# Performance work log

Hardware: AMD Instinct MI355X
Metric: run time of the kernel (lower is better)

Reference implementation:

```python
import jax, jax.numpy as jnp
import numpy as np

N, E, H, HEADS = 50000, 800000, 64, 4
EPS = 1e-5
NEG_SLOPE = 0.2


def _ln(x, g, b):
    mu = x.mean(-1, keepdims=True)
    var = x.var(-1, keepdims=True)
    return (x - mu) / jnp.sqrt(var + EPS) * g + b


def _gat(x, row, col, W, a_src, a_dst, bias, heads, out_dim, concat):
    # PyG GATConv: add self-loops, linear, per-edge attention, segment softmax, scatter-agg
    n = x.shape[0]
    loop = jnp.arange(n, dtype=row.dtype)
    r = jnp.concatenate([row, loop])  # message sources
    c = jnp.concatenate([col, loop])  # message targets (aggregation index)
    h = (x @ W).reshape(n, heads, out_dim)              # [N, heads, out]
    a_s = jnp.sum(h * a_src, axis=-1)                   # [N, heads]
    a_d = jnp.sum(h * a_dst, axis=-1)                   # [N, heads]
    e = jax.nn.leaky_relu(a_s[r] + a_d[c], NEG_SLOPE)   # [E', heads]
    m = jax.ops.segment_max(e, c, num_segments=n)       # stable softmax per target node
    p = jnp.exp(e - m[c])
    alpha = p / jax.ops.segment_sum(p, c, num_segments=n)[c]
    out = jax.ops.segment_sum(h[r] * alpha[..., None], c, num_segments=n)  # [N, heads, out]
    out = out.reshape(n, heads * out_dim) if concat else out.mean(axis=1)
    return out + bias


def setup_inputs() -> dict:
    key = jax.random.key(0)
    ks = jax.random.split(key, 16)
    d = {}
    d["node_embeds"] = jax.random.normal(ks[0], (N, H), jnp.float32)
    d["edge_index"] = jax.random.randint(ks[1], (2, E), 0, N, jnp.int32)
    d["edge_embeds"] = jax.random.normal(ks[2], (E, H), jnp.float32)
    layer_cfg = [(H, HEADS, H, True), (H * HEADS, HEADS, H, True), (H * HEADS, 1, H, False)]
    i = 3
    for li, (din, heads, dout, concat) in enumerate(layer_cfg):
        d[f"W{li}"] = jax.random.normal(ks[i], (din, heads * dout), jnp.float32) * 0.05; i += 1
        d[f"asrc{li}"] = jax.random.normal(ks[i], (heads, dout), jnp.float32) * 0.05; i += 1
        d[f"adst{li}"] = jax.random.normal(ks[i], (heads, dout), jnp.float32) * 0.05; i += 1
        odim = heads * dout if concat else dout
        d[f"b{li}"] = jnp.zeros((odim,), jnp.float32)
        d[f"g{li}"] = jnp.ones((odim,), jnp.float32)
        d[f"be{li}"] = jnp.zeros((odim,), jnp.float32)
    return d


def reference(node_embeds, edge_index, edge_embeds,
              W0, asrc0, adst0, b0, g0, be0,
              W1, asrc1, adst1, b1, g1, be1,
              W2, asrc2, adst2, b2, g2, be2):
    row, col = edge_index[0], edge_index[1]
    # scatter-mean edge embeddings onto target nodes (reduce='mean', clamp count>=1)
    cnt = jnp.maximum(jax.ops.segment_sum(jnp.ones((E,), jnp.float32), col, num_segments=N), 1.0)
    x = node_embeds + jax.ops.segment_sum(edge_embeds, col, num_segments=N) / cnt[:, None]
    layers = [
        (W0, asrc0, adst0, b0, g0, be0, HEADS, True),
        (W1, asrc1, adst1, b1, g1, be1, HEADS, True),
        (W2, asrc2, adst2, b2, g2, be2, 1, False),
    ]
    for (W, a_s, a_d, b, g, be, heads, concat) in layers:
        x = _gat(x, row, col, W, a_s, a_d, b, heads, H, concat)
        x = jax.nn.elu(_ln(x, g, be))
        # dropout: identity in eval mode
    return x
```

## Files before the change

kernel.cpp:

```cpp
#include <hip/hip_runtime.h>
#include <math.h>

#define NN 50000
#define NE 800000
#define MPAD 50048
#define NB 196

typedef __attribute__((ext_vector_type(8))) short bf16x8;
typedef __attribute__((ext_vector_type(8))) unsigned short u16x8;
typedef __attribute__((ext_vector_type(4))) float f32x4;

__device__ __forceinline__ float leaky(float x){ return x > 0.f ? x : 0.2f*x; }

__device__ __forceinline__ unsigned short f2bf(float f){
  unsigned int u = __float_as_uint(f);
  unsigned int r = (u + 0x7fffu + ((u >> 16) & 1u)) >> 16;
  return (unsigned short)r;
}
__device__ __forceinline__ float bf2f(unsigned short u){
  return __uint_as_float(((unsigned int)u) << 16);
}

__global__ void k_zero(int* __restrict__ deg,
                       float* __restrict__ AS0, float* __restrict__ AD0,
                       float* __restrict__ AS1, float* __restrict__ AD1,
                       float* __restrict__ AS2, float* __restrict__ AD2){
  int i = blockIdx.x*blockDim.x + threadIdx.x;
  if (i < NN) deg[i] = 0;
  if (i < NN*4){
    AS0[i]=0.f; AD0[i]=0.f;
    AS1[i]=0.f; AD1[i]=0.f;
    AS2[i]=0.f; AD2[i]=0.f;
  }
}

__global__ void k_hist(const int* __restrict__ col, int* __restrict__ deg){
  int e = blockIdx.x*blockDim.x + threadIdx.x;
  if (e < NE) atomicAdd(&deg[col[e]], 1);
}

__global__ void k_scan1(const int* __restrict__ deg, int* __restrict__ off,
                        int* __restrict__ bsum){
  __shared__ int ws[4];
  int t = threadIdx.x;
  int i = blockIdx.x*256 + t;
  int v = (i<NN)? deg[i] : 0;
  int lane = t & 63, w = t >> 6;
  int x = v;
  #pragma unroll
  for (int d=1; d<64; d<<=1){
    int y = __shfl_up(x, d, 64);
    if (lane >= d) x += y;
  }
  if (lane==63) ws[w] = x;
  __syncthreads();
  int woff = 0;
  #pragma unroll
  for (int k=0;k<3;++k) if (k < w) woff += ws[k];
  int incl = x + woff;
  if (i<NN) off[i] = incl - v;
  if (t==255) bsum[blockIdx.x] = incl;
}

__global__ void k_scan2(int* __restrict__ bsum, int* __restrict__ off){
  __shared__ int ws[4];
  int t = threadIdx.x;
  int v = (t<NB)? bsum[t] : 0;
  int lane = t & 63, w = t >> 6;
  int x = v;
  #pragma unroll
  for (int d=1; d<64; d<<=1){
    int y = __shfl_up(x, d, 64);
    if (lane >= d) x += y;
  }
  if (lane==63) ws[w] = x;
  __syncthreads();
  int woff = 0;
  #pragma unroll
  for (int k=0;k<3;++k) if (k < w) woff += ws[k];
  int incl = x + woff;
  if (t<NB) bsum[t] = incl - v;
  if (t==NB-1) off[NN] = incl;
}

__global__ void k_scan3(const int* __restrict__ bsum, int* __restrict__ off,
                        int* __restrict__ cursor){
  int i = blockIdx.x*256 + threadIdx.x;
  if (i<NN){
    int v = off[i] + bsum[blockIdx.x];
    off[i] = v;
    cursor[i] = v;
  }
}

__global__ void k_scatter(const int* __restrict__ row, const int* __restrict__ col,
                          int* __restrict__ cursor, int* __restrict__ esrc, int* __restrict__ eid){
  int e = blockIdx.x*blockDim.x + threadIdx.x;
  if (e < NE){
    int c = col[e];
    int pos = atomicAdd(&cursor[c], 1);
    esrc[pos] = row[e];
    eid[pos]  = e;
  }
}

__global__ void k_premix(const float* __restrict__ node, const float* __restrict__ ee,
                         const int* __restrict__ off, const int* __restrict__ eid,
                         unsigned short* __restrict__ Xb){
  int wid  = (int)((blockIdx.x*blockDim.x + threadIdx.x) >> 6);
  int lane = threadIdx.x & 63;
  if (wid >= NN) return;
  int g  = lane >> 3;
  int l8 = lane & 7;
  int s0 = off[wid], s1 = off[wid+1];

  float a[8];
  #pragma unroll
  for (int v=0;v<8;++v) a[v]=0.f;
  for (int p = s0 + g; p < s1; p += 8){
    int ed = eid[p];
    const float4* rp = reinterpret_cast<const float4*>(ee + (size_t)ed*64 + l8*8);
    float4 h0 = rp[0], h1 = rp[1];
    a[0]+=h0.x; a[1]+=h0.y; a[2]+=h0.z; a[3]+=h0.w;
    a[4]+=h1.x; a[5]+=h1.y; a[6]+=h1.z; a[7]+=h1.w;
  }
  #pragma unroll
  for (int mk=8; mk<64; mk<<=1){
    #pragma unroll
    for (int v=0;v<8;++v) a[v] += __shfl_xor(a[v], mk, 64);
  }
  if (lane < 8){
    int dcnt = s1 - s0;
    float c = 1.f/(float)(dcnt > 1 ? dcnt : 1);
    const float4* np = reinterpret_cast<const float4*>(node + (size_t)wid*64 + l8*8);
    float4 n0 = np[0], n1 = np[1];
    float nv[8] = {n0.x,n0.y,n0.z,n0.w,n1.x,n1.y,n1.z,n1.w};
    u16x8 o;
    #pragma unroll
    for (int v=0;v<8;++v) o[v] = f2bf(nv[v] + a[v]*c);
    *reinterpret_cast<u16x8*>(Xb + (size_t)wid*64 + l8*8) = o;
  }
}

__global__ void k_wconv(const float* __restrict__ W, unsigned short* __restrict__ Wt,
                        int K, int Ncols){
  int idx = blockIdx.x*blockDim.x + threadIdx.x;
  if (idx < K*Ncols){
    int n = idx / K, k = idx - n*K;
    Wt[idx] = f2bf(W[(size_t)k*Ncols + n]);
  }
}

template<int BN, int K, int HEADS>
__global__ __launch_bounds__(256)
void k_gemm_mfma(const unsigned short* __restrict__ A,
                 const unsigned short* __restrict__ Bt,
                 unsigned short* __restrict__ C,
                 const float* __restrict__ asrc, const float* __restrict__ adst,
                 float* __restrict__ AS, float* __restrict__ AD, int Nc){
  constexpr int BM = 128, BK = 32;
  constexpr int WNT = BN/32;
  __shared__ __align__(16) unsigned short As[BM*BK];
  __shared__ __align__(16) unsigned short Bs[BN*BK];
  const int tid  = threadIdx.x;
  const int lane = tid & 63;
  const int wid  = tid >> 6;
  const int wr   = wid >> 1, wc = wid & 1;
  const int bm   = blockIdx.y * BM, bn = blockIdx.x * BN;
  const int r    = lane >> 2, kq = lane & 3;

  f32x4 acc[4][WNT];
  #pragma unroll
  for (int i=0;i<4;++i)
    #pragma unroll
    for (int j=0;j<WNT;++j) acc[i][j] = (f32x4){0.f,0.f,0.f,0.f};

  for (int k0=0; k0<K; k0+=BK){
    #pragma unroll
    for (int i=0;i<2;++i){
      int arow = wid*32 + i*16 + r;
      __builtin_amdgcn_global_load_lds(
        (const __attribute__((address_space(1))) void*)(A + (size_t)(bm+arow)*K + k0 + kq*8),
        (__attribute__((address_space(3))) void*)&As[(wid*32 + i*16)*BK],
        16, 0, 0);
    }
    #pragma unroll
    for (int i=0;i<BN/64;++i){
      int brow = wid*(BN/4) + i*16 + r;
      __builtin_amdgcn_global_load_lds(
        (const __attribute__((address_space(1))) void*)(Bt + (size_t)(bn+brow)*K + k0 + kq*8),
        (__attribute__((address_space(3))) void*)&Bs[(wid*(BN/4) + i*16)*BK],
        16, 0, 0);
    }
    __syncthreads();

    bf16x8 af[4], bfr[WNT];
    #pragma unroll
    for (int mi=0; mi<4; ++mi)
      af[mi] = *reinterpret_cast<const bf16x8*>(&As[(wr*64 + mi*16 + (lane&15))*BK + (lane>>4)*8]);
    #pragma unroll
    for (int ni=0; ni<WNT; ++ni)
      bfr[ni] = *reinterpret_cast<const bf16x8*>(&Bs[(wc*(BN/2) + ni*16 + (lane&15))*BK + (lane>>4)*8]);
    #pragma unroll
    for (int mi=0; mi<4; ++mi)
      #pragma unroll
      for (int ni=0; ni<WNT; ++ni)
        acc[mi][ni] = __builtin_amdgcn_mfma_f32_16x16x32_bf16(af[mi], bfr[ni], acc[mi][ni], 0, 0, 0);
    __syncthreads();
  }

  const int head = (bn + wc*(BN/2)) >> 6;
  float av[WNT], dv[WNT];
  #pragma unroll
  for (int ni=0; ni<WNT; ++ni){
    int ccol = bn + wc*(BN/2) + ni*16 + (lane&15);
    av[ni] = asrc[ccol];
    dv[ni] = adst[ccol];
  }

  #pragma unroll
  for (int mi=0; mi<4; ++mi){
    #pragma unroll
    for (int ni=0; ni<WNT; ++ni){
      int ccol = bn + wc*(BN/2) + ni*16 + (lane&15);
      int rbase = bm + wr*64 + mi*16 + (lane>>4)*4;
      #pragma unroll
      for (int reg=0; reg<4; ++reg)
        C[(size_t)(rbase+reg)*Nc + ccol] = f2bf(acc[mi][ni][reg]);
    }
    float sp[4] = {0.f,0.f,0.f,0.f}, dp[4] = {0.f,0.f,0.f,0.f};
    #pragma unroll
    for (int ni=0; ni<WNT; ++ni)
      #pragma unroll
      for (int reg=0; reg<4; ++reg){
        sp[reg] += acc[mi][ni][reg]*av[ni];
        dp[reg] += acc[mi][ni][reg]*dv[ni];
      }
    #pragma unroll
    for (int reg=0; reg<4; ++reg)
      #pragma unroll
      for (int mk=1; mk<16; mk<<=1){
        sp[reg] += __shfl_xor(sp[reg], mk, 64);
        dp[reg] += __shfl_xor(dp[reg], mk, 64);
      }
    if ((lane & 15) == 0){
      int rr = bm + wr*64 + mi*16 + (lane>>4)*4;
      #pragma unroll
      for (int reg=0; reg<4; ++reg){
        atomicAdd(&AS[(size_t)(rr+reg)*HEADS + head], sp[reg]);
        atomicAdd(&AD[(size_t)(rr+reg)*HEADS + head], dp[reg]);
      }
    }
  }
}

template<int HEADS, bool OUT_BF16>
__global__ void k_agg(const unsigned short* __restrict__ Hb, const float* __restrict__ AS,
                      const float* __restrict__ AD, const int* __restrict__ off,
                      const int* __restrict__ esrc,
                      const float* __restrict__ bias, const float* __restrict__ gamma,
                      const float* __restrict__ beta, void* __restrict__ OutP){
  constexpr int D  = HEADS*64;
  constexpr int L  = (HEADS==4) ? 16 : 8;
  constexpr int C  = D / L;
  constexpr int NG = 64 / L;
  constexpr int NV = C / 8;
  int wid  = (int)((blockIdx.x*blockDim.x + threadIdx.x) >> 6);
  int lane = threadIdx.x & 63;
  if (wid >= NN) return;
  const int g    = lane / L;
  const int lrow = lane & (L-1);
  const int col0 = lrow * C;
  const int head = col0 >> 6;

  float ad    = AD[(size_t)wid*HEADS + head];
  float wself = leaky(AS[(size_t)wid*HEADS + head] + ad);
  int s0 = off[wid], s1 = off[wid+1];

  float m, psum;
  float acc[C];
  if (g == 0){
    m = wself; psum = 1.f;
    const u16x8* hp = reinterpret_cast<const u16x8*>(Hb + (size_t)wid*D + col0);
    u16x8 hv[NV];
    #pragma unroll
    for (int q=0;q<NV;++q) hv[q] = hp[q];
    #pragma unroll
    for (int v=0;v<C;++v) acc[v] = bf2f((unsigned short)hv[v>>3][v&7]);
  } else {
    m = -1e30f; psum = 0.f;
    #pragma unroll
    for (int v=0;v<C;++v) acc[v]=0.f;
  }

  for (int p = s0 + g; p < s1; p += NG){
    int src = esrc[p];
    float w = leaky(AS[(size_t)src*HEADS + head] + ad);
    float mn = fmaxf(m, w);
    float scale = __expf(m - mn);
    float pw    = __expf(w - mn);
    m = mn;
    psum = psum*scale + pw;
    const u16x8* hp = reinterpret_cast<const u16x8*>(Hb + (size_t)src*D + col0);
    u16x8 hv[NV];
    #pragma unroll
    for (int q=0;q<NV;++q) hv[q] = hp[q];
    #pragma unroll
    for (int v=0;v<C;++v) acc[v] = acc[v]*scale + pw*bf2f((unsigned short)hv[v>>3][v&7]);
  }

  #pragma unroll
  for (int mk=L; mk<64; mk<<=1){
    float m_o    = __shfl_xor(m, mk, 64);
    float psum_o = __shfl_xor(psum, mk, 64);
    float mn = fmaxf(m, m_o);
    float sA = __expf(m - mn);
    float sB = __expf(m_o - mn);
    psum = psum*sA + psum_o*sB;
    #pragma unroll
    for (int v=0;v<C;++v){
      float a_o = __shfl_xor(acc[v], mk, 64);
      acc[v] = acc[v]*sA + a_o*sB;
    }
    m = mn;
  }

  float inv = 1.f/psum;
  float val[C];
  float s=0.f, s2=0.f;
  #pragma unroll
  for (int v=0;v<C;++v){
    val[v] = acc[v]*inv + bias[col0+v];
    s  += val[v];
    s2 += val[v]*val[v];
  }
  #pragma unroll
  for (int mk=1; mk<64; mk<<=1){
    s  += __shfl_xor(s,  mk, 64);
    s2 += __shfl_xor(s2, mk, 64);
  }
  float mean = s/(float)(64*C);
  float var  = s2/(float)(64*C) - mean*mean;
  float rstd = rsqrtf(var + 1e-5f);
  if (g == 0){
    if constexpr (OUT_BF16){
      u16x8 o[NV];
      #pragma unroll
      for (int v=0;v<C;++v){
        float y = (val[v]-mean)*rstd*gamma[col0+v] + beta[col0+v];
        y = (y > 0.f) ? y : expm1f(y);
        o[v>>3][v&7] = f2bf(y);
      }
      u16x8* op = reinterpret_cast<u16x8*>((unsigned short*)OutP + (size_t)wid*D + col0);
      #pragma unroll
      for (int q=0;q<NV;++q) op[q] = o[q];
    } else {
      float o[C];
      #pragma unroll
      for (int v=0;v<C;++v){
        float y = (val[v]-mean)*rstd*gamma[col0+v] + beta[col0+v];
        o[v] = (y > 0.f) ? y : expm1f(y);
      }
      float4* op = reinterpret_cast<float4*>((float*)OutP + (size_t)wid*D + col0);
      #pragma unroll
      for (int q=0;q<C/4;++q){
        float4 o4 = {o[q*4+0],o[q*4+1],o[q*4+2],o[q*4+3]};
        op[q] = o4;
      }
    }
  }
}

extern "C" void kernel_launch(void* const* d_in, const int* in_sizes, int n_in,
                              void* d_out, int out_size, void* d_ws, size_t ws_size,
                              hipStream_t stream) {
  const float* node  = (const float*)d_in[0];
  const int*   eidx  = (const int*)d_in[1];
  const float* ee    = (const float*)d_in[2];
  const float* W0    = (const float*)d_in[3];
  const float* asrc0 = (const float*)d_in[4];
  const float* adst0 = (const float*)d_in[5];
  const float* b0    = (const float*)d_in[6];
  const float* g0    = (const float*)d_in[7];
  const float* be0   = (const float*)d_in[8];
  const float* W1    = (const float*)d_in[9];
  const float* asrc1 = (const float*)d_in[10];
  const float* adst1 = (const float*)d_in[11];
  const float* b1    = (const float*)d_in[12];
  const float* g1    = (const float*)d_in[13];
  const float* be1   = (const float*)d_in[14];
  const float* W2    = (const float*)d_in[15];
  const float* asrc2 = (const float*)d_in[16];
  const float* adst2 = (const float*)d_in[17];
  const float* b2    = (const float*)d_in[18];
  const float* g2    = (const float*)d_in[19];
  const float* be2   = (const float*)d_in[20];

  const int* row = eidx;
  const int* col = eidx + NE;

  unsigned short* Hb  = (unsigned short*)d_ws;
  unsigned short* Xb0 = Hb  + (size_t)MPAD*256;
  unsigned short* Xb  = Xb0 + (size_t)MPAD*64;
  unsigned short* Wt0 = Xb  + (size_t)MPAD*256;
  unsigned short* Wt1 = Wt0 + 256*64;
  unsigned short* Wt2 = Wt1 + 256*256;
  float* AS0 = (float*)(Wt2 + 64*256);
  float* AD0 = AS0 + (size_t)MPAD*4;
  float* AS1 = AD0 + (size_t)MPAD*4;
  float* AD1 = AS1 + (size_t)MPAD*4;
  float* AS2 = AD1 + (size_t)MPAD*4;
  float* AD2 = AS2 + (size_t)MPAD*4;
  int* deg   = (int*)(AD2 + (size_t)MPAD*4);
  int* off   = deg + NN;
  int* cursor= off + NN + 1;
  int* esrc  = cursor + NN;
  int* eid   = esrc + NE;
  int* bsum  = eid + NE;

  float* out = (float*)d_out;

  k_zero<<<(NN*4+255)/256, 256, 0, stream>>>(deg, AS0, AD0, AS1, AD1, AS2, AD2);
  k_hist<<<(NE+255)/256, 256, 0, stream>>>(col, deg);
  k_scan1<<<NB, 256, 0, stream>>>(deg, off, bsum);
  k_scan2<<<1, 256, 0, stream>>>(bsum, off);
  k_scan3<<<NB, 256, 0, stream>>>(bsum, off, cursor);
  k_scatter<<<(NE+255)/256, 256, 0, stream>>>(row, col, cursor, esrc, eid);

  k_wconv<<<(256*64 +255)/256, 256, 0, stream>>>(W0, Wt0, 64, 256);
  k_wconv<<<(256*256+255)/256, 256, 0, stream>>>(W1, Wt1, 256, 256);
  k_wconv<<<(64*256 +255)/256, 256, 0, stream>>>(W2, Wt2, 256, 64);

  int nwaveblk = (NN*64 + 255)/256;
  k_premix<<<nwaveblk, 256, 0, stream>>>(node, ee, off, eid, Xb0);

  {
    dim3 g(256/128, MPAD/128);
    k_gemm_mfma<128,64,4><<<g, 256, 0, stream>>>(Xb0, Wt0, Hb, asrc0, adst0, AS0, AD0, 256);
    k_agg<4,true><<<nwaveblk, 256, 0, stream>>>(Hb, AS0, AD0, off, esrc, b0, g0, be0, Xb);
  }
  {
    dim3 g(256/128, MPAD/128);
    k_gemm_mfma<128,256,4><<<g, 256, 0, stream>>>(Xb, Wt1, Hb, asrc1, adst1, AS1, AD1, 256);
    k_agg<4,true><<<nwaveblk, 256, 0, stream>>>(Hb, AS1, AD1, off, esrc, b1, g1, be1, Xb);
  }
  {
    dim3 g(64/64, MPAD/128);
    k_gemm_mfma<64,256,1><<<g, 256, 0, stream>>>(Xb, Wt2, Hb, asrc2, adst2, AS2, AD2, 64);
    k_agg<1,false><<<nwaveblk, 256, 0, stream>>>(Hb, AS2, AD2, off, esrc, b2, g2, be2, out);
  }
}
```

Before: 497.3 us.

## Precompute per-node softmax max in a pre-pass; drop online rescaling in aggregation

Adds a first pass in which the whole wave reads neighbor attention scores and reduces the per-head max. The main loop then accumulates exp(w-m) directly, with no running rescale, and the cross-group merge becomes a plain shuffle-add. It also halves lanes per row (L 16->8 and 8->4), so each lane holds more columns and more edge groups run in parallel. This costs an extra read of esrc and AS per node, and the wider per-lane accumulators raise register pressure.

```diff
diff --git a/kernel.cpp b/kernel.cpp
--- a/kernel.cpp
+++ b/kernel.cpp
@@ -261,7 +261,7 @@
                       const float* __restrict__ bias, const float* __restrict__ gamma,
                       const float* __restrict__ beta, void* __restrict__ OutP){
   constexpr int D  = HEADS*64;
-  constexpr int L  = (HEADS==4) ? 16 : 8;
+  constexpr int L  = (HEADS==4) ? 8 : 4;
   constexpr int C  = D / L;
   constexpr int NG = 64 / L;
   constexpr int NV = C / 8;
@@ -273,56 +273,82 @@
   const int col0 = lrow * C;
   const int head = col0 >> 6;
 
+  int s0 = off[wid], s1 = off[wid+1];
+
+  float m;
+  if constexpr (HEADS==4){
+    float4 ad4 = *reinterpret_cast<const float4*>(AD + (size_t)wid*4);
+    float4 as4 = *reinterpret_cast<const float4*>(AS + (size_t)wid*4);
+    float mx0 = leaky(as4.x+ad4.x), mx1 = leaky(as4.y+ad4.y);
+    float mx2 = leaky(as4.z+ad4.z), mx3 = leaky(as4.w+ad4.w);
+    for (int p = s0 + lane; p < s1; p += 64){
+      int src = esrc[p];
+      float4 a4 = *reinterpret_cast<const float4*>(AS + (size_t)src*4);
+      mx0 = fmaxf(mx0, leaky(a4.x+ad4.x));
+      mx1 = fmaxf(mx1, leaky(a4.y+ad4.y));
+      mx2 = fmaxf(mx2, leaky(a4.z+ad4.z));
+      mx3 = fmaxf(mx3, leaky(a4.w+ad4.w));
+    }
+    #pragma unroll
+    for (int mk=1; mk<64; mk<<=1){
+      mx0 = fmaxf(mx0, __shfl_xor(mx0, mk, 64));
+      mx1 = fmaxf(mx1, __shfl_xor(mx1, mk, 64));
+      mx2 = fmaxf(mx2, __shfl_xor(mx2, mk, 64));
+      mx3 = fmaxf(mx3, __shfl_xor(mx3, mk, 64));
+    }
+    float m01 = (head & 1) ? mx1 : mx0;
+    float m23 = (head & 1) ? mx3 : mx2;
+    m = (head & 2) ? m23 : m01;
+  } else {
+    float ad0 = AD[wid];
+    float mx0 = leaky(AS[wid]+ad0);
+    for (int p = s0 + lane; p < s1; p += 64){
+      int src = esrc[p];
+      mx0 = fmaxf(mx0, leaky(AS[src]+ad0));
+    }
+    #pragma unroll
+    for (int mk=1; mk<64; mk<<=1)
+      mx0 = fmaxf(mx0, __shfl_xor(mx0, mk, 64));
+    m = mx0;
+  }
+
   float ad    = AD[(size_t)wid*HEADS + head];
   float wself = leaky(AS[(size_t)wid*HEADS + head] + ad);
-  int s0 = off[wid], s1 = off[wid+1];
-
-  float m, psum;
+
+  float psum = 0.f;
   float acc[C];
+  #pragma unroll
+  for (int v=0;v<C;++v) acc[v]=0.f;
+
   if (g == 0){
-    m = wself; psum = 1.f;
+    float pw = __expf(wself - m);
+    psum = pw;
     const u16x8* hp = reinterpret_cast<const u16x8*>(Hb + (size_t)wid*D + col0);
     u16x8 hv[NV];
     #pragma unroll
     for (int q=0;q<NV;++q) hv[q] = hp[q];
     #pragma unroll
-    for (int v=0;v<C;++v) acc[v] = bf2f((unsigned short)hv[v>>3][v&7]);
-  } else {
-    m = -1e30f; psum = 0.f;
-    #pragma unroll
-    for (int v=0;v<C;++v) acc[v]=0.f;
+    for (int v=0;v<C;++v) acc[v] = pw*bf2f((unsigned short)hv[v>>3][v&7]);
   }
 
   for (int p = s0 + g; p < s1; p += NG){
     int src = esrc[p];
-    float w = leaky(AS[(size_t)src*HEADS + head] + ad);
-    float mn = fmaxf(m, w);
-    float scale = __expf(m - mn);
-    float pw    = __expf(w - mn);
-    m = mn;
-    psum = psum*scale + pw;
+    float w  = leaky(AS[(size_t)src*HEADS + head] + ad);
+    float pw = __expf(w - m);
+    psum += pw;
     const u16x8* hp = reinterpret_cast<const u16x8*>(Hb + (size_t)src*D + col0);
     u16x8 hv[NV];
     #pragma unroll
     for (int q=0;q<NV;++q) hv[q] = hp[q];
     #pragma unroll
-    for (int v=0;v<C;++v) acc[v] = acc[v]*scale + pw*bf2f((unsigned short)hv[v>>3][v&7]);
+    for (int v=0;v<C;++v) acc[v] += pw*bf2f((unsigned short)hv[v>>3][v&7]);
   }
 
   #pragma unroll
   for (int mk=L; mk<64; mk<<=1){
-    float m_o    = __shfl_xor(m, mk, 64);
-    float psum_o = __shfl_xor(psum, mk, 64);
-    float mn = fmaxf(m, m_o);
-    float sA = __expf(m - mn);
-    float sB = __expf(m_o - mn);
-    psum = psum*sA + psum_o*sB;
-    #pragma unroll
-    for (int v=0;v<C;++v){
-      float a_o = __shfl_xor(acc[v], mk, 64);
-      acc[v] = acc[v]*sA + a_o*sB;
-    }
-    m = mn;
+    psum += __shfl_xor(psum, mk, 64);
+    #pragma unroll
+    for (int v=0;v<C;++v) acc[v] += __shfl_xor(acc[v], mk, 64);
   }
 
   float inv = 1.f/psum;
```

After: 679.2 us. +36.6%, slower.
